# Performance work log

Measured on AMD Instinct MI355X. Metric: run time of the kernel, lower is better.

The kernel has to match this reference:

```python
import jax, jax.numpy as jnp
import numpy as np

N = 100000          # number of nodes (nums)
E = 1200000         # nnz of the normalized adjacency
D = 64              # embed_size; layer_size = [64, 64, 64]
NODE_DROP = 0.1     # args.node_dropout[0]
MESS_DROP = (0.1, 0.1, 0.1)
EPS = 1e-12         # F.normalize eps


def setup_inputs() -> dict:
    key = jax.random.key(0)
    ks = jax.random.split(key, 10)
    rows = jax.random.randint(ks[0], (E,), 0, N, dtype=jnp.int32)
    cols = jax.random.randint(ks[1], (E,), 0, N, dtype=jnp.int32)
    vals = jax.random.uniform(ks[2], (E,), dtype=jnp.float32)
    emb = jax.random.normal(ks[3], (N, D), dtype=jnp.float32) * 0.1
    W0 = jax.random.normal(ks[4], (D, D), dtype=jnp.float32) * 0.1
    b0 = jax.random.normal(ks[5], (1, D), dtype=jnp.float32) * 0.1
    W1 = jax.random.normal(ks[6], (D, D), dtype=jnp.float32) * 0.1
    b1 = jax.random.normal(ks[7], (1, D), dtype=jnp.float32) * 0.1
    W2 = jax.random.normal(ks[8], (D, D), dtype=jnp.float32) * 0.1
    b2 = jax.random.normal(ks[9], (1, D), dtype=jnp.float32) * 0.1
    return dict(rows=rows, cols=cols, vals=vals, emb=emb,
                W0=W0, b0=b0, W1=W1, b1=b1, W2=W2, b2=b2)


def reference(rows, cols, vals, emb, W0, b0, W1, b1, W2, b2):
    drop_key = jax.random.key(42)
    k_node, k0, k1, k2 = jax.random.split(drop_key, 4)

    # sparse node dropout: zero dropped edge values (== removing nnz), scale survivors
    keep_e = jax.random.bernoulli(k_node, 1.0 - NODE_DROP, (E,))
    a_vals = jnp.where(keep_e, vals / (1.0 - NODE_DROP), 0.0)

    def layer(ego, W, b, rate, k):
        # SpMM: out[r] += a_vals * ego[c]   (COO scatter-add)
        side = jax.ops.segment_sum(a_vals[:, None] * ego[cols], rows, num_segments=N)
        h = side @ W + b
        keep = jax.random.bernoulli(k, 1.0 - rate, h.shape)
        h = jnp.where(keep, h / (1.0 - rate), 0.0)          # mess dropout
        nrm = h / jnp.maximum(jnp.linalg.norm(h, axis=1, keepdims=True), EPS)
        return h, nrm  # ego continues as the (un-normalized) dropped output

    all_embs = [emb]
    ego = emb
    for (W, b, rate, k) in ((W0, b0, MESS_DROP[0], k0),
                            (W1, b1, MESS_DROP[1], k1),
                            (W2, b2, MESS_DROP[2], k2)):
        ego, nrm = layer(ego, W, b, rate, k)
        all_embs.append(nrm)
    return jnp.concatenate(all_embs, axis=1)  # [N, 4*D]
```

## Files before the change

### kernel.cpp

```cpp
#include <hip/hip_runtime.h>
#include <stdint.h>

#define N_NODES 100000
#define DIM 64
#define E_EDGES 1200000
#define RPB 16
#define NB 6250
#define BCAP 288
#define ROW_CAP 40
#define BPB 16

__host__ __device__ __forceinline__ void tf2x32(uint32_t k0, uint32_t k1,
                                                uint32_t c0, uint32_t c1,
                                                uint32_t& o0, uint32_t& o1) {
    uint32_t ks2 = k0 ^ k1 ^ 0x1BD11BDAu;
    uint32_t x0 = c0 + k0, x1 = c1 + k1;
#define TF_RND(r) { x0 += x1; x1 = (x1 << r) | (x1 >> (32 - r)); x1 ^= x0; }
    TF_RND(13) TF_RND(15) TF_RND(26) TF_RND(6)
    x0 += k1;  x1 += ks2 + 1u;
    TF_RND(17) TF_RND(29) TF_RND(16) TF_RND(24)
    x0 += ks2; x1 += k0 + 2u;
    TF_RND(13) TF_RND(15) TF_RND(26) TF_RND(6)
    x0 += k0;  x1 += k1 + 3u;
    TF_RND(17) TF_RND(29) TF_RND(16) TF_RND(24)
    x0 += k1;  x1 += ks2 + 4u;
    TF_RND(13) TF_RND(15) TF_RND(26) TF_RND(6)
    x0 += ks2; x1 += k0 + 5u;
#undef TF_RND
    o0 = x0; o1 = x1;
}

__device__ __forceinline__ bool keep_bit(uint32_t k0, uint32_t k1, uint32_t idx) {
    uint32_t y0, y1;
    tf2x32(k0, k1, 0u, idx, y0, y1);
    return (((y0 ^ y1) >> 9) < 7549747u);
}

__device__ __forceinline__ uint16_t f2bf(float f) {
    uint32_t x = __float_as_uint(f);
    return (uint16_t)((x + 0x7fffu + ((x >> 16) & 1u)) >> 16);
}

__global__ void k_bucket(const int* __restrict__ rows, const int* __restrict__ cols,
                         const float* __restrict__ vals, int* __restrict__ bcnt,
                         int2* __restrict__ bedge, uint32_t k0, uint32_t k1) {
    int i = blockIdx.x * blockDim.x + threadIdx.x;
    int stride = gridDim.x * blockDim.x;
    for (; i < E_EDGES; i += stride) {
        if (keep_bit(k0, k1, (uint32_t)i)) {
            int r = rows[i];
            int b = r >> 4;
            int rl = r & (RPB - 1);
            int pos = atomicAdd(&bcnt[b], 1);
            if (pos < BCAP)
                bedge[(size_t)b * BCAP + pos] =
                    make_int2((rl << 17) | cols[i],
                              __float_as_int(vals[i] * (1.0f / 0.9f)));
        }
    }
}

__global__ __launch_bounds__(256) void k_bin(const int2* __restrict__ bedge,
                                             const int* __restrict__ bcnt,
                                             uint32_t* __restrict__ pairs,
                                             int* __restrict__ cnt) {
    __shared__ uint32_t lp[256 * ROW_CAP];
    __shared__ int lc[256];
    int blk = blockIdx.x, t = threadIdx.x;
    for (int i = t; i < 256 * ROW_CAP / 4; i += 256)
        ((uint4*)lp)[i] = make_uint4(0u, 0u, 0u, 0u);
    lc[t] = 0;
    __syncthreads();
    int b0 = blk * BPB;
    int nb = NB - b0; if (nb > BPB) nb = BPB;
    for (int lb = 0; lb < nb; ++lb) {
        int bb = b0 + lb;
        int ne = bcnt[bb];
        if (ne > BCAP) ne = BCAP;
        const int2* be = bedge + (size_t)bb * BCAP;
        for (int e = t; e < ne; e += 256) {
            int2 en = be[e];
            uint32_t meta = (uint32_t)en.x;
            int rl = (int)(meta >> 17);
            uint32_t col = meta & 0x1FFFFu;
            float v = __int_as_float(en.y);
            int rloc = lb * RPB + rl;
            int pos = atomicAdd(&lc[rloc], 1);
            if (pos < ROW_CAP) {
                uint32_t q = (uint32_t)(v * 16384.0f + 0.5f);
                lp[rloc * ROW_CAP + pos] = (q << 17) | col;
            }
        }
    }
    __syncthreads();
    int nrows = N_NODES - blk * 256;
    if (nrows > 256) nrows = 256;
    int nq = nrows * ROW_CAP / 4;
    uint4* dst = (uint4*)(pairs + (size_t)blk * 256 * ROW_CAP);
    const uint4* src = (const uint4*)lp;
    for (int i = t; i < nq; i += 256) dst[i] = src[i];
    if (t < nrows) cnt[blk * 256 + t] = lc[t];
}

__global__ void k_embcvt(const float* __restrict__ emb, float* __restrict__ out,
                         uint16_t* __restrict__ egoA) {
    int i = blockIdx.x * blockDim.x + threadIdx.x;
    int stride = gridDim.x * blockDim.x;
    const int total = N_NODES * 16;
    for (; i < total; i += stride) {
        int n = i >> 4, q = i & 15;
        float4 v = ((const float4*)emb)[(size_t)n * 16 + q];
        ((float4*)out)[(size_t)n * 64 + q] = v;
        ushort4 bb;
        bb.x = f2bf(v.x); bb.y = f2bf(v.y); bb.z = f2bf(v.z); bb.w = f2bf(v.w);
        ((ushort4*)egoA)[(size_t)n * 16 + q] = bb;
    }
}

__global__ __launch_bounds__(256) void k_layer(
    const int* __restrict__ cnt, const uint32_t* __restrict__ pairs,
    const uint16_t* __restrict__ ego_in,
    uint16_t* __restrict__ h_out,
    float* __restrict__ out, int coloff,
    const float* __restrict__ W, const float* __restrict__ bias,
    uint32_t k0, uint32_t k1) {
    __shared__ float sW[64 * 64];
    __shared__ float sb[64];
    __shared__ float sS[4][64];
    int t = threadIdx.x;
    for (int i = t; i < 1024; i += 256)
        ((float4*)sW)[i] = ((const float4*)W)[i];
    if (t < 16)
        ((float4*)sb)[t] = ((const float4*)bias)[t];
    __syncthreads();

    const float S = 1.0f / 16384.0f;
    int w = t >> 6, lane = t & 63;
    int l2 = lane & 31;
    int hi4 = (lane >> 5) << 2;
    const uint32_t* egoU = (const uint32_t*)ego_in;
    int wid0 = blockIdx.x * 4 + w;
    const int NW = 2048 * 4;
    for (int n = wid0; n < N_NODES; n += NW) {
        int un = __builtin_amdgcn_readfirstlane(n);
        int len = (cnt[un] + 7) & ~7;
        if (len > ROW_CAP) len = ROW_CAP;
        const uint32_t* rowp = pairs + (size_t)un * ROW_CAP + hi4;
        float accE = 0.f, accO = 0.f;
        for (int j = 0; j < len; j += 8) {
            uint4 V = *reinterpret_cast<const uint4*>(rowp + j);
            uint32_t c0 = V.x & 0x1FFFFu;  float a0 = (float)(V.x >> 17) * S;
            uint32_t c1 = V.y & 0x1FFFFu;  float a1 = (float)(V.y >> 17) * S;
            uint32_t c2 = V.z & 0x1FFFFu;  float a2 = (float)(V.z >> 17) * S;
            uint32_t c3 = V.w & 0x1FFFFu;  float a3 = (float)(V.w >> 17) * S;
            uint32_t u0 = egoU[c0 * 32u + (uint32_t)l2];
            uint32_t u1 = egoU[c1 * 32u + (uint32_t)l2];
            uint32_t u2 = egoU[c2 * 32u + (uint32_t)l2];
            uint32_t u3 = egoU[c3 * 32u + (uint32_t)l2];
            accE = fmaf(a0, __uint_as_float(u0 << 16), accE);
            accO = fmaf(a0, __uint_as_float(u0 & 0xffff0000u), accO);
            accE = fmaf(a1, __uint_as_float(u1 << 16), accE);
            accO = fmaf(a1, __uint_as_float(u1 & 0xffff0000u), accO);
            accE = fmaf(a2, __uint_as_float(u2 << 16), accE);
            accO = fmaf(a2, __uint_as_float(u2 & 0xffff0000u), accO);
            accE = fmaf(a3, __uint_as_float(u3 << 16), accE);
            accO = fmaf(a3, __uint_as_float(u3 & 0xffff0000u), accO);
        }
        accE += __shfl_xor(accE, 32, 64);
        accO += __shfl_xor(accO, 32, 64);
        if (lane < 32)
            reinterpret_cast<float2*>(&sS[w][0])[l2] = make_float2(accE, accO);
        float h = sb[lane];
        const float4* s4p = reinterpret_cast<const float4*>(&sS[w][0]);
#pragma unroll
        for (int kq = 0; kq < 16; ++kq) {
            float4 s4 = s4p[kq];
            h = fmaf(s4.x, sW[(4 * kq + 0) * 64 + lane], h);
            h = fmaf(s4.y, sW[(4 * kq + 1) * 64 + lane], h);
            h = fmaf(s4.z, sW[(4 * kq + 2) * 64 + lane], h);
            h = fmaf(s4.w, sW[(4 * kq + 3) * 64 + lane], h);
        }
        uint32_t idx = (uint32_t)un * 64u + (uint32_t)lane;
        h = keep_bit(k0, k1, idx) ? h / 0.9f : 0.0f;
        float s = h * h;
#pragma unroll
        for (int o = 32; o > 0; o >>= 1) s += __shfl_xor(s, o, 64);
        float nv = h / fmaxf(sqrtf(s), 1e-12f);
        if (h_out) h_out[(size_t)n * DIM + lane] = f2bf(h);
        out[(size_t)n * 256 + coloff + lane] = nv;
    }
}

extern "C" void kernel_launch(void* const* d_in, const int* in_sizes, int n_in,
                              void* d_out, int out_size, void* d_ws, size_t ws_size,
                              hipStream_t stream) {
    const int*   rows = (const int*)d_in[0];
    const int*   cols = (const int*)d_in[1];
    const float* vals = (const float*)d_in[2];
    const float* emb  = (const float*)d_in[3];
    const float* Wk[3] = { (const float*)d_in[4], (const float*)d_in[6], (const float*)d_in[8] };
    const float* bk[3] = { (const float*)d_in[5], (const float*)d_in[7], (const float*)d_in[9] };
    float* out = (float*)d_out;

    int*      bcnt  = (int*)d_ws;
    int*      cnt   = bcnt + 8192;
    int2*     bedge = (int2*)((char*)d_ws + 32768 + 400000);
    uint32_t* pairs = (uint32_t*)(bedge + (size_t)NB * BCAP);
    uint16_t* egoA  = (uint16_t*)(pairs + (size_t)N_NODES * ROW_CAP);
    uint16_t* egoB  = egoA + (size_t)N_NODES * DIM;

    uint32_t kn[2], kl[3][2];
    tf2x32(0u, 42u, 0u, 0u, kn[0], kn[1]);
    tf2x32(0u, 42u, 0u, 1u, kl[0][0], kl[0][1]);
    tf2x32(0u, 42u, 0u, 2u, kl[1][0], kl[1][1]);
    tf2x32(0u, 42u, 0u, 3u, kl[2][0], kl[2][1]);

    hipMemsetAsync(bcnt, 0, 8192 * 4, stream);
    k_bucket<<<2048, 256, 0, stream>>>(rows, cols, vals, bcnt, bedge, kn[0], kn[1]);
    k_bin<<<(NB + BPB - 1) / BPB, 256, 0, stream>>>(bedge, bcnt, pairs, cnt);
    k_embcvt<<<2048, 256, 0, stream>>>(emb, out, egoA);

    k_layer<<<2048, 256, 0, stream>>>(cnt, pairs, egoA, egoB, out, 64,
                                      Wk[0], bk[0], kl[0][0], kl[0][1]);
    k_layer<<<2048, 256, 0, stream>>>(cnt, pairs, egoB, egoA, out, 128,
                                      Wk[1], bk[1], kl[1][0], kl[1][1]);
    k_layer<<<2048, 256, 0, stream>>>(cnt, pairs, egoA, nullptr, out, 192,
                                      Wk[2], bk[2], kl[2][0], kl[2][1]);
}
```

Baseline: 281.5 us.

## Precompute dropout masks in prep kernel and hold W in registers

Moves the three per-layer message-dropout Threefry computations out of the layer kernels into the embedding-conversion kernel, which stores them as per-node 64-bit ballot masks that each layer reads with a single load. The weight matrix is now held in 64 registers per lane instead of LDS, launch bounds are set to 4 blocks per SM, and the bucket capacity is reduced. The aim is to take the RNG work off the latency-bound SpMM kernels, at the cost of extra register pressure that may limit occupancy, a prep kernel that now works on scalar floats instead of float4, and a smaller bucket capacity that leaves less slack against overflow.

Measured after the change: 311.4 us. 1.11x slower.

```diff
diff --git a/kernel.cpp b/kernel.cpp
--- a/kernel.cpp
+++ b/kernel.cpp
@@ -6,7 +6,7 @@
 #define E_EDGES 1200000
 #define RPB 16
 #define NB 6250
-#define BCAP 288
+#define BCAP 264
 #define ROW_CAP 40
 #define BPB 16
 
@@ -102,40 +102,48 @@
     if (t < nrows) cnt[blk * 256 + t] = lc[t];
 }
 
-__global__ void k_embcvt(const float* __restrict__ emb, float* __restrict__ out,
-                         uint16_t* __restrict__ egoA) {
-    int i = blockIdx.x * blockDim.x + threadIdx.x;
-    int stride = gridDim.x * blockDim.x;
-    const int total = N_NODES * 16;
-    for (; i < total; i += stride) {
-        int n = i >> 4, q = i & 15;
-        float4 v = ((const float4*)emb)[(size_t)n * 16 + q];
-        ((float4*)out)[(size_t)n * 64 + q] = v;
-        ushort4 bb;
-        bb.x = f2bf(v.x); bb.y = f2bf(v.y); bb.z = f2bf(v.z); bb.w = f2bf(v.w);
-        ((ushort4*)egoA)[(size_t)n * 16 + q] = bb;
-    }
-}
-
-__global__ __launch_bounds__(256) void k_layer(
+__global__ void k_prep(const float* __restrict__ emb, float* __restrict__ out,
+                       uint16_t* __restrict__ egoA, uint64_t* __restrict__ masks,
+                       uint32_t k10, uint32_t k11, uint32_t k20, uint32_t k21,
+                       uint32_t k30, uint32_t k31) {
+    int gid = blockIdx.x * blockDim.x + threadIdx.x;
+    int lane = threadIdx.x & 63;
+    int wid = gid >> 6;
+    int nw = (gridDim.x * blockDim.x) >> 6;
+    for (int n = wid; n < N_NODES; n += nw) {
+        float v = emb[(size_t)n * DIM + lane];
+        out[(size_t)n * 256 + lane] = v;
+        egoA[(size_t)n * DIM + lane] = f2bf(v);
+        uint32_t idx = (uint32_t)n * 64u + (uint32_t)lane;
+        uint64_t m0 = __ballot(keep_bit(k10, k11, idx));
+        uint64_t m1 = __ballot(keep_bit(k20, k21, idx));
+        uint64_t m2 = __ballot(keep_bit(k30, k31, idx));
+        if (lane == 0) {
+            masks[n] = m0;
+            masks[N_NODES + n] = m1;
+            masks[2 * N_NODES + n] = m2;
+        }
+    }
+}
+
+__global__ __launch_bounds__(256, 4) void k_layer(
     const int* __restrict__ cnt, const uint32_t* __restrict__ pairs,
     const uint16_t* __restrict__ ego_in,
     uint16_t* __restrict__ h_out,
     float* __restrict__ out, int coloff,
     const float* __restrict__ W, const float* __restrict__ bias,
-    uint32_t k0, uint32_t k1) {
-    __shared__ float sW[64 * 64];
-    __shared__ float sb[64];
+    const uint64_t* __restrict__ lmask) {
     __shared__ float sS[4][64];
     int t = threadIdx.x;
-    for (int i = t; i < 1024; i += 256)
-        ((float4*)sW)[i] = ((const float4*)W)[i];
-    if (t < 16)
-        ((float4*)sb)[t] = ((const float4*)bias)[t];
-    __syncthreads();
+    int w = t >> 6, lane = t & 63;
+
+    float wreg[64];
+#pragma unroll
+    for (int k = 0; k < 64; ++k)
+        wreg[k] = W[k * 64 + lane];
+    float breg = bias[lane];
 
     const float S = 1.0f / 16384.0f;
-    int w = t >> 6, lane = t & 63;
     int l2 = lane & 31;
     int hi4 = (lane >> 5) << 2;
     const uint32_t* egoU = (const uint32_t*)ego_in;
@@ -170,18 +178,18 @@
         accO += __shfl_xor(accO, 32, 64);
         if (lane < 32)
             reinterpret_cast<float2*>(&sS[w][0])[l2] = make_float2(accE, accO);
-        float h = sb[lane];
+        float h = breg;
         const float4* s4p = reinterpret_cast<const float4*>(&sS[w][0]);
 #pragma unroll
         for (int kq = 0; kq < 16; ++kq) {
             float4 s4 = s4p[kq];
-            h = fmaf(s4.x, sW[(4 * kq + 0) * 64 + lane], h);
-            h = fmaf(s4.y, sW[(4 * kq + 1) * 64 + lane], h);
-            h = fmaf(s4.z, sW[(4 * kq + 2) * 64 + lane], h);
-            h = fmaf(s4.w, sW[(4 * kq + 3) * 64 + lane], h);
-        }
-        uint32_t idx = (uint32_t)un * 64u + (uint32_t)lane;
-        h = keep_bit(k0, k1, idx) ? h / 0.9f : 0.0f;
+            h = fmaf(s4.x, wreg[4 * kq + 0], h);
+            h = fmaf(s4.y, wreg[4 * kq + 1], h);
+            h = fmaf(s4.z, wreg[4 * kq + 2], h);
+            h = fmaf(s4.w, wreg[4 * kq + 3], h);
+        }
+        uint64_t m = lmask[un];
+        h = ((m >> lane) & 1ull) ? h * (1.0f / 0.9f) : 0.0f;
         float s = h * h;
 #pragma unroll
         for (int o = 32; o > 0; o >>= 1) s += __shfl_xor(s, o, 64);
@@ -204,7 +212,8 @@
 
     int*      bcnt  = (int*)d_ws;
     int*      cnt   = bcnt + 8192;
-    int2*     bedge = (int2*)((char*)d_ws + 32768 + 400000);
+    uint64_t* masks = (uint64_t*)((char*)d_ws + 32768 + 400000);
+    int2*     bedge = (int2*)(masks + 3 * N_NODES);
     uint32_t* pairs = (uint32_t*)(bedge + (size_t)NB * BCAP);
     uint16_t* egoA  = (uint16_t*)(pairs + (size_t)N_NODES * ROW_CAP);
     uint16_t* egoB  = egoA + (size_t)N_NODES * DIM;
@@ -218,12 +227,14 @@
     hipMemsetAsync(bcnt, 0, 8192 * 4, stream);
     k_bucket<<<2048, 256, 0, stream>>>(rows, cols, vals, bcnt, bedge, kn[0], kn[1]);
     k_bin<<<(NB + BPB - 1) / BPB, 256, 0, stream>>>(bedge, bcnt, pairs, cnt);
-    k_embcvt<<<2048, 256, 0, stream>>>(emb, out, egoA);
+    k_prep<<<2048, 256, 0, stream>>>(emb, out, egoA, masks,
+                                     kl[0][0], kl[0][1], kl[1][0], kl[1][1],
+                                     kl[2][0], kl[2][1]);
 
     k_layer<<<2048, 256, 0, stream>>>(cnt, pairs, egoA, egoB, out, 64,
-                                      Wk[0], bk[0], kl[0][0], kl[0][1]);
+                                      Wk[0], bk[0], masks);
     k_layer<<<2048, 256, 0, stream>>>(cnt, pairs, egoB, egoA, out, 128,
-                                      Wk[1], bk[1], kl[1][0], kl[1][1]);
+                                      Wk[1], bk[1], masks + N_NODES);
     k_layer<<<2048, 256, 0, stream>>>(cnt, pairs, egoA, nullptr, out, 192,
-                                      Wk[2], bk[2], kl[2][0], kl[2][1]);
-}
+                                      Wk[2], bk[2], masks + 2 * N_NODES);
+}
```

## Process two nodes per wave and keep W column in registers

Applied to the files above, without the earlier changes.

Each wave now handles two adjacent nodes per iteration and interleaves their gather loops, exposing more independent memory loads. The 64x64 weight matrix moves from shared memory into 64 per-lane registers, which removes the block-wide barrier and the LDS reads of W. The bucket capacity BCAP is also reduced. The costs are higher register pressure under launch_bounds(256,4), which may limit occupancy, and wasted gather work when the two row lengths differ. A smaller BCAP also risks overflowing buckets.

After: 237.5 us. 1.19x faster.

```diff
diff --git a/kernel.cpp b/kernel.cpp
--- a/kernel.cpp
+++ b/kernel.cpp
@@ -6,7 +6,7 @@
 #define E_EDGES 1200000
 #define RPB 16
 #define NB 6250
-#define BCAP 288
+#define BCAP 264
 #define ROW_CAP 40
 #define BPB 16
 
@@ -117,77 +117,107 @@
     }
 }
 
-__global__ __launch_bounds__(256) void k_layer(
+#define GATHER_FMA(V, aE, aO)                                              \
+    {                                                                      \
+        uint32_t c0 = V.x & 0x1FFFFu;  float a0 = (float)(V.x >> 17) * S;  \
+        uint32_t c1 = V.y & 0x1FFFFu;  float a1 = (float)(V.y >> 17) * S;  \
+        uint32_t c2 = V.z & 0x1FFFFu;  float a2 = (float)(V.z >> 17) * S;  \
+        uint32_t c3 = V.w & 0x1FFFFu;  float a3 = (float)(V.w >> 17) * S;  \
+        uint32_t u0 = egoU[c0 * 32u + (uint32_t)l2];                       \
+        uint32_t u1 = egoU[c1 * 32u + (uint32_t)l2];                       \
+        uint32_t u2 = egoU[c2 * 32u + (uint32_t)l2];                       \
+        uint32_t u3 = egoU[c3 * 32u + (uint32_t)l2];                       \
+        aE = fmaf(a0, __uint_as_float(u0 << 16), aE);                      \
+        aO = fmaf(a0, __uint_as_float(u0 & 0xffff0000u), aO);              \
+        aE = fmaf(a1, __uint_as_float(u1 << 16), aE);                      \
+        aO = fmaf(a1, __uint_as_float(u1 & 0xffff0000u), aO);              \
+        aE = fmaf(a2, __uint_as_float(u2 << 16), aE);                      \
+        aO = fmaf(a2, __uint_as_float(u2 & 0xffff0000u), aO);              \
+        aE = fmaf(a3, __uint_as_float(u3 << 16), aE);                      \
+        aO = fmaf(a3, __uint_as_float(u3 & 0xffff0000u), aO);              \
+    }
+
+__global__ __launch_bounds__(256, 4) void k_layer(
     const int* __restrict__ cnt, const uint32_t* __restrict__ pairs,
     const uint16_t* __restrict__ ego_in,
     uint16_t* __restrict__ h_out,
     float* __restrict__ out, int coloff,
     const float* __restrict__ W, const float* __restrict__ bias,
     uint32_t k0, uint32_t k1) {
-    __shared__ float sW[64 * 64];
-    __shared__ float sb[64];
-    __shared__ float sS[4][64];
+    __shared__ float sS[8][64];
     int t = threadIdx.x;
-    for (int i = t; i < 1024; i += 256)
-        ((float4*)sW)[i] = ((const float4*)W)[i];
-    if (t < 16)
-        ((float4*)sb)[t] = ((const float4*)bias)[t];
-    __syncthreads();
+    int w = t >> 6, lane = t & 63;
+
+    float wreg[64];
+#pragma unroll
+    for (int k = 0; k < 64; ++k)
+        wreg[k] = W[k * 64 + lane];
+    float breg = bias[lane];
 
     const float S = 1.0f / 16384.0f;
-    int w = t >> 6, lane = t & 63;
     int l2 = lane & 31;
     int hi4 = (lane >> 5) << 2;
     const uint32_t* egoU = (const uint32_t*)ego_in;
     int wid0 = blockIdx.x * 4 + w;
     const int NW = 2048 * 4;
-    for (int n = wid0; n < N_NODES; n += NW) {
-        int un = __builtin_amdgcn_readfirstlane(n);
-        int len = (cnt[un] + 7) & ~7;
-        if (len > ROW_CAP) len = ROW_CAP;
-        const uint32_t* rowp = pairs + (size_t)un * ROW_CAP + hi4;
-        float accE = 0.f, accO = 0.f;
-        for (int j = 0; j < len; j += 8) {
-            uint4 V = *reinterpret_cast<const uint4*>(rowp + j);
-            uint32_t c0 = V.x & 0x1FFFFu;  float a0 = (float)(V.x >> 17) * S;
-            uint32_t c1 = V.y & 0x1FFFFu;  float a1 = (float)(V.y >> 17) * S;
-            uint32_t c2 = V.z & 0x1FFFFu;  float a2 = (float)(V.z >> 17) * S;
-            uint32_t c3 = V.w & 0x1FFFFu;  float a3 = (float)(V.w >> 17) * S;
-            uint32_t u0 = egoU[c0 * 32u + (uint32_t)l2];
-            uint32_t u1 = egoU[c1 * 32u + (uint32_t)l2];
-            uint32_t u2 = egoU[c2 * 32u + (uint32_t)l2];
-            uint32_t u3 = egoU[c3 * 32u + (uint32_t)l2];
-            accE = fmaf(a0, __uint_as_float(u0 << 16), accE);
-            accO = fmaf(a0, __uint_as_float(u0 & 0xffff0000u), accO);
-            accE = fmaf(a1, __uint_as_float(u1 << 16), accE);
-            accO = fmaf(a1, __uint_as_float(u1 & 0xffff0000u), accO);
-            accE = fmaf(a2, __uint_as_float(u2 << 16), accE);
-            accO = fmaf(a2, __uint_as_float(u2 & 0xffff0000u), accO);
-            accE = fmaf(a3, __uint_as_float(u3 << 16), accE);
-            accO = fmaf(a3, __uint_as_float(u3 & 0xffff0000u), accO);
-        }
-        accE += __shfl_xor(accE, 32, 64);
-        accO += __shfl_xor(accO, 32, 64);
-        if (lane < 32)
-            reinterpret_cast<float2*>(&sS[w][0])[l2] = make_float2(accE, accO);
-        float h = sb[lane];
-        const float4* s4p = reinterpret_cast<const float4*>(&sS[w][0]);
+    const int NPAIR = N_NODES / 2;
+    for (int nn = wid0; nn < NPAIR; nn += NW) {
+        int un0 = __builtin_amdgcn_readfirstlane(nn * 2);
+        int un1 = un0 + 1;
+        int len0 = (cnt[un0] + 7) & ~7;  if (len0 > ROW_CAP) len0 = ROW_CAP;
+        int len1 = (cnt[un1] + 7) & ~7;  if (len1 > ROW_CAP) len1 = ROW_CAP;
+        const uint32_t* rowp0 = pairs + (size_t)un0 * ROW_CAP + hi4;
+        const uint32_t* rowp1 = pairs + (size_t)un1 * ROW_CAP + hi4;
+        float accE0 = 0.f, accO0 = 0.f, accE1 = 0.f, accO1 = 0.f;
+        int jmax = len0 > len1 ? len0 : len1;
+        for (int j = 0; j < jmax; j += 8) {
+            uint4 V0 = (j < len0) ? *reinterpret_cast<const uint4*>(rowp0 + j)
+                                  : make_uint4(0u, 0u, 0u, 0u);
+            uint4 V1 = (j < len1) ? *reinterpret_cast<const uint4*>(rowp1 + j)
+                                  : make_uint4(0u, 0u, 0u, 0u);
+            GATHER_FMA(V0, accE0, accO0)
+            GATHER_FMA(V1, accE1, accO1)
+        }
+        accE0 += __shfl_xor(accE0, 32, 64);
+        accO0 += __shfl_xor(accO0, 32, 64);
+        accE1 += __shfl_xor(accE1, 32, 64);
+        accO1 += __shfl_xor(accO1, 32, 64);
+        if (lane < 32) {
+            reinterpret_cast<float2*>(&sS[2 * w][0])[l2] = make_float2(accE0, accO0);
+            reinterpret_cast<float2*>(&sS[2 * w + 1][0])[l2] = make_float2(accE1, accO1);
+        }
+        float h0 = breg, h1 = breg;
+        const float4* s4p0 = reinterpret_cast<const float4*>(&sS[2 * w][0]);
+        const float4* s4p1 = reinterpret_cast<const float4*>(&sS[2 * w + 1][0]);
 #pragma unroll
         for (int kq = 0; kq < 16; ++kq) {
-            float4 s4 = s4p[kq];
-            h = fmaf(s4.x, sW[(4 * kq + 0) * 64 + lane], h);
-            h = fmaf(s4.y, sW[(4 * kq + 1) * 64 + lane], h);
-            h = fmaf(s4.z, sW[(4 * kq + 2) * 64 + lane], h);
-            h = fmaf(s4.w, sW[(4 * kq + 3) * 64 + lane], h);
-        }
-        uint32_t idx = (uint32_t)un * 64u + (uint32_t)lane;
-        h = keep_bit(k0, k1, idx) ? h / 0.9f : 0.0f;
-        float s = h * h;
+            float4 s40 = s4p0[kq];
+            float4 s41 = s4p1[kq];
+            h0 = fmaf(s40.x, wreg[4 * kq + 0], h0);
+            h1 = fmaf(s41.x, wreg[4 * kq + 0], h1);
+            h0 = fmaf(s40.y, wreg[4 * kq + 1], h0);
+            h1 = fmaf(s41.y, wreg[4 * kq + 1], h1);
+            h0 = fmaf(s40.z, wreg[4 * kq + 2], h0);
+            h1 = fmaf(s41.z, wreg[4 * kq + 2], h1);
+            h0 = fmaf(s40.w, wreg[4 * kq + 3], h0);
+            h1 = fmaf(s41.w, wreg[4 * kq + 3], h1);
+        }
+        h0 = keep_bit(k0, k1, (uint32_t)un0 * 64u + (uint32_t)lane) ? h0 * (1.0f / 0.9f) : 0.0f;
+        h1 = keep_bit(k0, k1, (uint32_t)un1 * 64u + (uint32_t)lane) ? h1 * (1.0f / 0.9f) : 0.0f;
+        float s0 = h0 * h0, s1 = h1 * h1;
 #pragma unroll
-        for (int o = 32; o > 0; o >>= 1) s += __shfl_xor(s, o, 64);
-        float nv = h / fmaxf(sqrtf(s), 1e-12f);
-        if (h_out) h_out[(size_t)n * DIM + lane] = f2bf(h);
-        out[(size_t)n * 256 + coloff + lane] = nv;
+        for (int o = 32; o > 0; o >>= 1) {
+            s0 += __shfl_xor(s0, o, 64);
+            s1 += __shfl_xor(s1, o, 64);
+        }
+        float nv0 = h0 / fmaxf(sqrtf(s0), 1e-12f);
+        float nv1 = h1 / fmaxf(sqrtf(s1), 1e-12f);
+        if (h_out) {
+            h_out[(size_t)un0 * DIM + lane] = f2bf(h0);
+            h_out[(size_t)un1 * DIM + lane] = f2bf(h1);
+        }
+        out[(size_t)un0 * 256 + coloff + lane] = nv0;
+        out[(size_t)un1 * 256 + coloff + lane] = nv1;
     }
 }
 
```
